# Performance work log

Measured on AMD Instinct MI355X. Metric: run time of the kernel, lower is better.

Reference implementation:

```python
import jax, jax.numpy as jnp
import numpy as np

HIDDEN = 2048
NUM_HEADS = 16
HEAD_DIM = HIDDEN // NUM_HEADS  # 128
LATENT = HIDDEN // 8            # 256
ROPE_THETA = 100000.0


def setup_inputs() -> dict:
    key = jax.random.key(0)
    ks = jax.random.split(key, 7)
    s = 0.02
    x = jax.random.normal(ks[0], (4, 1024, HIDDEN), dtype=jnp.float32)
    # weights stored as [in, out] (transpose of torch nn.Linear.weight)
    w_q_down = jax.random.normal(ks[1], (HIDDEN, LATENT), dtype=jnp.float32) * s
    w_kv_down = jax.random.normal(ks[2], (HIDDEN, LATENT), dtype=jnp.float32) * s
    w_q_up = jax.random.normal(ks[3], (LATENT, HIDDEN), dtype=jnp.float32) * s
    w_k_up = jax.random.normal(ks[4], (LATENT, HIDDEN), dtype=jnp.float32) * s
    w_v_up = jax.random.normal(ks[5], (LATENT, HIDDEN), dtype=jnp.float32) * s
    w_o = jax.random.normal(ks[6], (HIDDEN, HIDDEN), dtype=jnp.float32) * s
    return {"x": x, "w_q_down": w_q_down, "w_kv_down": w_kv_down,
            "w_q_up": w_q_up, "w_k_up": w_k_up, "w_v_up": w_v_up, "w_o": w_o}


def _rope_cos_sin(seq_len, dtype):
    # Llama rotary: inv_freq over even dims, emb = concat(freqs, freqs)
    inv_freq = 1.0 / (ROPE_THETA ** (jnp.arange(0, HEAD_DIM, 2, dtype=jnp.float32) / HEAD_DIM))
    pos = jnp.arange(seq_len, dtype=jnp.float32)
    freqs = pos[:, None] * inv_freq[None, :]          # [S, D/2]
    emb = jnp.concatenate([freqs, freqs], axis=-1)    # [S, D]
    return jnp.cos(emb).astype(dtype), jnp.sin(emb).astype(dtype)


def _rotate_half(t):
    h = t.shape[-1] // 2
    return jnp.concatenate([-t[..., h:], t[..., :h]], axis=-1)


def reference(x, w_q_down, w_kv_down, w_q_up, w_k_up, w_v_up, w_o):
    B, S, H = x.shape
    q_latent = x @ w_q_down                 # [B,S,latent]
    kv_latent = x @ w_kv_down               # [B,S,latent]
    q = (q_latent @ w_q_up).reshape(B, S, NUM_HEADS, HEAD_DIM)
    k = (kv_latent @ w_k_up).reshape(B, S, NUM_HEADS, HEAD_DIM)
    v = (kv_latent @ w_v_up).reshape(B, S, NUM_HEADS, HEAD_DIM)

    cos, sin = _rope_cos_sin(S, x.dtype)    # [S,D]
    cos = cos[None, :, None, :]             # [1,S,1,D] (unsqueeze_dim=2)
    sin = sin[None, :, None, :]
    q = q * cos + _rotate_half(q) * sin
    k = k * cos + _rotate_half(k) * sin

    # [B,H,S,D]
    q = q.transpose(0, 2, 1, 3)
    k = k.transpose(0, 2, 1, 3)
    v = v.transpose(0, 2, 1, 3)

    scale = 1.0 / jnp.sqrt(jnp.asarray(HEAD_DIM, dtype=x.dtype))
    scores = jnp.einsum('bhqd,bhkd->bhqk', q, k) * scale
    causal = jnp.tril(jnp.ones((S, S), dtype=bool))
    scores = jnp.where(causal[None, None], scores, jnp.finfo(scores.dtype).min)
    probs = jax.nn.softmax(scores, axis=-1)
    attn = jnp.einsum('bhqk,bhkd->bhqd', probs, v)  # [B,H,S,D]
    attn = attn.transpose(0, 2, 1, 3).reshape(B, S, H)
    return attn @ w_o
```

## Files before the change

kernel.cpp:

```cpp
#include <hip/hip_runtime.h>
#include <hip/hip_bf16.h>

typedef unsigned short u16;
typedef unsigned int u32;
typedef __attribute__((ext_vector_type(8))) __bf16 bf16x8;
typedef __attribute__((ext_vector_type(4))) float f32x4;

#define HID 2048
#define NH 16
#define HD 128
#define LAT 256
#define BATCH 4
#define SEQ 1024

__device__ __forceinline__ u16 f2bf(float f) {
  union { float f; u32 u; } v; v.f = f;
  u32 r = v.u + 0x7fffu + ((v.u >> 16) & 1u);
  return (u16)(r >> 16);
}

typedef const __attribute__((address_space(1))) u32 as1_u32;
typedef __attribute__((address_space(3))) u32 as3_u32;

__device__ __forceinline__ void load_lds16(const void* g, void* l) {
  __builtin_amdgcn_global_load_lds((as1_u32*)g, (as3_u32*)l, 16, 0, 0);
}

template<int WM, int WN, int MR, int NR>
__device__ __forceinline__ void gemm_core(const u16* __restrict__ A, const u16* __restrict__ Bt,
    int K, int lda, int ldb, int arow0, int brow0, u16* As, u16* Bs, f32x4 acc[MR][NR]) {
  constexpr int BM = WM * MR * 16, BN = WN * NR * 16;
  constexpr int NW = WM * WN;
  constexpr int ACH = (BM * 32) / 512;
  constexpr int BCH = (BN * 32) / 512;
  const int tid = threadIdx.x;
  const int lane = tid & 63, wave = tid >> 6;
  const int wm = wave % WM, wn = wave / WM;
  const int fr = lane & 15, fq = lane >> 4;

  for (int kt = 0; kt < K; kt += 32) {
    __syncthreads();
    #pragma unroll
    for (int cc = 0; cc < ACH / NW; ++cc) {
      int c = wave + cc * NW;
      int r = c * 16 + (lane >> 2);
      int col = (lane & 3) * 8;
      load_lds16(&A[(size_t)(arow0 + r) * lda + kt + col], &As[c * 512]);
    }
    #pragma unroll
    for (int cc = 0; cc < BCH / NW; ++cc) {
      int c = wave + cc * NW;
      int r = c * 16 + (lane >> 2);
      int col = (lane & 3) * 8;
      load_lds16(&Bt[(size_t)(brow0 + r) * ldb + kt + col], &Bs[c * 512]);
    }
    asm volatile("s_waitcnt vmcnt(0)" ::: "memory");
    __syncthreads();
    bf16x8 af[MR], bfr[NR];
    #pragma unroll
    for (int m = 0; m < MR; ++m)
      af[m] = *(const bf16x8*)&As[(wm * MR * 16 + m * 16 + fr) * 32 + fq * 8];
    #pragma unroll
    for (int n = 0; n < NR; ++n)
      bfr[n] = *(const bf16x8*)&Bs[(wn * NR * 16 + n * 16 + fr) * 32 + fq * 8];
    #pragma unroll
    for (int m = 0; m < MR; ++m)
      #pragma unroll
      for (int n = 0; n < NR; ++n)
        acc[m][n] = __builtin_amdgcn_mfma_f32_16x16x32_bf16(af[m], bfr[n], acc[m][n], 0, 0, 0);
  }
}

__global__ void __launch_bounds__(256) k_cvt(const float* __restrict__ in, u16* __restrict__ o, int n4) {
  int i = blockIdx.x * blockDim.x + threadIdx.x;
  if (i < n4) {
    float4 v = ((const float4*)in)[i];
    union { u16 s[4]; uint2 u; } w;
    w.s[0] = f2bf(v.x); w.s[1] = f2bf(v.y); w.s[2] = f2bf(v.z); w.s[3] = f2bf(v.w);
    ((uint2*)o)[i] = w.u;
  }
}

__global__ void __launch_bounds__(256) k_transpose3(const float* __restrict__ in0,
    const float* __restrict__ in1, const float* __restrict__ in2,
    u16* __restrict__ o0, u16* __restrict__ o1, u16* __restrict__ o2, int R, int C) {
  __shared__ float t[32][33];
  const float* in = blockIdx.z == 0 ? in0 : (blockIdx.z == 1 ? in1 : in2);
  u16* o = blockIdx.z == 0 ? o0 : (blockIdx.z == 1 ? o1 : o2);
  int bx = blockIdx.x * 32, by = blockIdx.y * 32;
  int tx = threadIdx.x, ty = threadIdx.y;
  #pragma unroll
  for (int i = ty; i < 32; i += 8) t[i][tx] = in[(size_t)(by + i) * C + bx + tx];
  __syncthreads();
  #pragma unroll
  for (int i = ty; i < 32; i += 8) o[(size_t)(bx + i) * R + by + tx] = f2bf(t[tx][i]);
}

__global__ void __launch_bounds__(256) k_cossin(float* __restrict__ cosT, float* __restrict__ sinT) {
  int idx = blockIdx.x * 256 + threadIdx.x;
  int s = idx >> 6, d = idx & 63;
  float inv = powf(100000.0f, -(float)d / 64.0f);
  float a = (float)s * inv;
  cosT[idx] = cosf(a);
  sinT[idx] = sinf(a);
}

__global__ void __launch_bounds__(512, 2) k_down(const u16* __restrict__ xb, const u16* __restrict__ wqdT,
    const u16* __restrict__ wkvdT, u16* __restrict__ ql, u16* __restrict__ kvl) {
  __shared__ __align__(16) u16 As[2][128 * 128];
  __shared__ __align__(16) u16 Bs[2][64 * 128];
  const u16* Bt = blockIdx.z ? wkvdT : wqdT;
  u16* out = blockIdx.z ? kvl : ql;
  const int rb = blockIdx.x * 128, cb = blockIdx.y * 64;
  const int tid = threadIdx.x, lane = tid & 63, wave = tid >> 6;
  const int wm = wave & 3, wn = wave >> 2;
  const int fr = lane & 15, fq = lane >> 4;
  const char* Ab = (const char*)xb;
  const char* Bb = (const char*)Bt;
  f32x4 acc[2][2] = {};

  auto stage = [&](int buf, int s) {
    #pragma unroll
    for (int cc = 0; cc < 4; ++cc) {
      int c = wave * 4 + cc;
      int L = c * 1024 + lane * 16;
      int Ls = L ^ (((L >> 8) & 7) << 4);
      int r = Ls >> 8, colb = Ls & 255;
      load_lds16(Ab + (size_t)(rb + r) * 4096 + s * 256 + colb, (char*)As[buf] + c * 1024);
    }
    #pragma unroll
    for (int cc = 0; cc < 2; ++cc) {
      int c = wave * 2 + cc;
      int L = c * 1024 + lane * 16;
      int Ls = L ^ (((L >> 8) & 7) << 4);
      int r = Ls >> 8, colb = Ls & 255;
      load_lds16(Bb + (size_t)(cb + r) * 4096 + s * 256 + colb, (char*)Bs[buf] + c * 1024);
    }
  };

  stage(0, 0);
  int buf = 0;
  for (int s = 0; s < 16; ++s) {
    if (s + 1 < 16) {
      stage(buf ^ 1, s + 1);
      asm volatile("s_waitcnt vmcnt(6)" ::: "memory");
    } else {
      asm volatile("s_waitcnt vmcnt(0)" ::: "memory");
    }
    asm volatile("s_barrier" ::: "memory");

    #pragma unroll
    for (int kk = 0; kk < 4; ++kk) {
      bf16x8 af[2], bfr[2];
      #pragma unroll
      for (int m = 0; m < 2; ++m) {
        int r = wm * 32 + m * 16 + fr;
        af[m] = *(const bf16x8*)((const char*)As[buf] + ((r * 256 + kk * 64 + fq * 16) ^ ((r & 7) << 4)));
      }
      #pragma unroll
      for (int n = 0; n < 2; ++n) {
        int r = wn * 32 + n * 16 + fr;
        bfr[n] = *(const bf16x8*)((const char*)Bs[buf] + ((r * 256 + kk * 64 + fq * 16) ^ ((r & 7) << 4)));
      }
      #pragma unroll
      for (int m = 0; m < 2; ++m)
        #pragma unroll
        for (int n = 0; n < 2; ++n)
          acc[m][n] = __builtin_amdgcn_mfma_f32_16x16x32_bf16(af[m], bfr[n], acc[m][n], 0, 0, 0);
    }

    asm volatile("s_barrier" ::: "memory");
    buf ^= 1;
  }

  #pragma unroll
  for (int m = 0; m < 2; ++m)
    #pragma unroll
    for (int n = 0; n < 2; ++n)
      #pragma unroll
      for (int i = 0; i < 4; ++i)
        out[(size_t)(rb + wm * 32 + m * 16 + fq * 4 + i) * LAT + cb + wn * 32 + n * 16 + fr] =
            f2bf(acc[m][n][i]);
}

__global__ void __launch_bounds__(256) k_up(const u16* __restrict__ ql, const u16* __restrict__ kvl,
    const u16* __restrict__ wquT, const u16* __restrict__ wkuT, const u16* __restrict__ wvuT,
    u16* __restrict__ q, u16* __restrict__ k, u16* __restrict__ vt,
    const float* __restrict__ cosT, const float* __restrict__ sinT) {
  __shared__ __align__(16) u16 As[128 * 32];
  __shared__ __align__(16) u16 Bs[128 * 32];
  const int mode = blockIdx.z;
  const u16* A = (mode == 0) ? ql : kvl;
  const u16* Bt = (mode == 0) ? wquT : (mode == 1 ? wkuT : wvuT);
  const int rb = blockIdx.x * 128;
  const int h = blockIdx.y;
  f32x4 acc[2][8] = {};
  gemm_core<4, 1, 2, 8>(A, Bt, LAT, LAT, LAT, rb, h * HD, As, Bs, acc);
  const int lane = threadIdx.x & 63, wave = threadIdx.x >> 6;
  const int fr = lane & 15, fq = lane >> 4;
  if (mode == 2) {
    #pragma unroll
    for (int m = 0; m < 2; ++m)
      #pragma unroll
      for (int n = 0; n < 8; ++n)
        #pragma unroll
        for (int i = 0; i < 4; ++i) {
          int row = rb + wave * 32 + m * 16 + fq * 4 + i;
          int b = row >> 10, s = row & 1023;
          int sp = (s & ~63) | (((s & 15) << 2) | ((s >> 4) & 3));
          vt[(size_t)((b * NH + h) * HD + n * 16 + fr) * SEQ + sp] = f2bf(acc[m][n][i]);
        }
  } else {
    u16* dst = (mode == 0) ? q : k;
    const float scale = (mode == 0) ? 0.08838834764831845f * 1.4426950408889634f : 1.0f;
    #pragma unroll
    for (int m = 0; m < 2; ++m)
      #pragma unroll
      for (int i = 0; i < 4; ++i) {
        int row = rb + wave * 32 + m * 16 + fq * 4 + i;
        int b = row >> 10, s = row & 1023;
        size_t base = (size_t)((b * NH + h) * SEQ + s) * HD;
        #pragma unroll
        for (int j = 0; j < 4; ++j) {
          int dlo = j * 16 + fr;
          float c = cosT[s * 64 + dlo], sn = sinT[s * 64 + dlo];
          float x1 = acc[m][j][i], x2 = acc[m][j + 4][i];
          dst[base + dlo] = f2bf((x1 * c - x2 * sn) * scale);
          dst[base + dlo + 64] = f2bf((x2 * c + x1 * sn) * scale);
        }
      }
  }
}

__global__ void __launch_bounds__(256, 2) k_attn(const u16* __restrict__ Q, const u16* __restrict__ Kc,
    const u16* __restrict__ Vt, u16* __restrict__ O) {
  __shared__ __align__(16) u16 Ks[2][64 * 128];
  __shared__ __align__(16) u16 Vs[2][128 * 64];
  __shared__ __align__(16) u16 Ps[4][32 * 64];
  const int f = blockIdx.x;
  const int j = (f < 256) ? (7 - (f >> 6)) : ((f - 256) >> 6);
  const int bh = (f & 7) * 8 + ((f >> 3) & 7);
  const int h = bh & (NH - 1), b = bh >> 4;
  const int tid = threadIdx.x, lane = tid & 63, wave = tid >> 6;
  const int fr = lane & 15, fq = lane >> 4;
  const int qw = j * 128 + wave * 32;
  const size_t qkb = (size_t)bh * SEQ * HD;
  const char* Kbase = (const char*)Kc + qkb * 2;
  const char* Vbase = (const char*)Vt + (size_t)bh * HD * SEQ * 2;
  const int nkt = 2 * j + 2;

  auto stage = [&](int buf, int kt) {
    #pragma unroll
    for (int cc = 0; cc < 4; ++cc) {
      int c = wave * 4 + cc;
      int L = c * 1024 + lane * 16;
      int Lk = L ^ (((L >> 8) & 7) << 4);
      load_lds16(Kbase + (size_t)kt * 16384 + Lk, (char*)Ks[buf] + c * 1024);
      int Lv = L ^ (((L >> 7) & 7) << 4);
      int rv = Lv >> 7, colb = Lv & 127;
      load_lds16(Vbase + (size_t)rv * (SEQ * 2) + (size_t)kt * 128 + colb, (char*)Vs[buf] + c * 1024);
    }
  };

  bf16x8 ones;
  #pragma unroll
  for (int z = 0; z < 8; ++z) ones[z] = (__bf16)1.0f;

  bf16x8 qf[2][4];
  #pragma unroll
  for (int m = 0; m < 2; ++m)
    #pragma unroll
    for (int c = 0; c < 4; ++c)
      qf[m][c] = *(const bf16x8*)&Q[qkb + (size_t)(qw + m * 16 + fr) * HD + c * 32 + fq * 8];

  f32x4 ao[2][8] = {};
  f32x4 lacc[2] = {};

  stage(0, 0);

  int cur = 0;
  for (int t = 0; t < nkt; ++t) {
    if (t + 1 < nkt) {
      stage(cur ^ 1, t + 1);
      asm volatile("s_waitcnt vmcnt(8)" ::: "memory");
    } else {
      asm volatile("s_waitcnt vmcnt(0)" ::: "memory");
    }
    asm volatile("s_barrier" ::: "memory");

    const int k0 = t * 64;
    if (k0 <= qw + 31) {
      f32x4 sc[2][4] = {};
      __builtin_amdgcn_s_setprio(1);
      #pragma unroll
      for (int c = 0; c < 4; ++c)
        #pragma unroll
        for (int n = 0; n < 4; ++n) {
          int rr = n * 16 + fr;
          int off = (rr * 256 + c * 64 + fq * 16) ^ ((rr & 7) << 4);
          bf16x8 kf = *(const bf16x8*)((const char*)Ks[cur] + off);
          #pragma unroll
          for (int m = 0; m < 2; ++m)
            sc[m][n] = __builtin_amdgcn_mfma_f32_16x16x32_bf16(qf[m][c], kf, sc[m][n], 0, 0, 0);
        }
      __builtin_amdgcn_s_setprio(0);

      bf16x8 pa[2][2];
      #pragma unroll
      for (int m = 0; m < 2; ++m) {
        const bool needmask = (k0 + 63 > qw + m * 16);
        #pragma unroll
        for (int i = 0; i < 4; ++i) {
          int row = qw + m * 16 + fq * 4 + i;
          float p[4];
          #pragma unroll
          for (int n = 0; n < 4; ++n) {
            float sv = sc[m][n][i];
            if (needmask) sv = (k0 + n * 16 + fr <= row) ? sv : -1e30f;
            p[n] = exp2f(sv);
          }
          u32 w0, w1;
          asm("v_cvt_pk_bf16_f32 %0, %1, %2" : "=v"(w0) : "v"(p[0]), "v"(p[1]));
          asm("v_cvt_pk_bf16_f32 %0, %1, %2" : "=v"(w1) : "v"(p[2]), "v"(p[3]));
          int prow = m * 16 + fq * 4 + i;
          int o = (prow * 128 + fr * 8) ^ ((prow & 7) << 4);
          *(uint2*)((char*)Ps[wave] + o) = make_uint2(w0, w1);
        }
        #pragma unroll
        for (int kf = 0; kf < 2; ++kf) {
          int rr = m * 16 + fr;
          int off = (rr * 128 + kf * 64 + fq * 16) ^ ((rr & 7) << 4);
          pa[m][kf] = *(const bf16x8*)((const char*)Ps[wave] + off);
        }
      }

      __builtin_amdgcn_s_setprio(1);
      #pragma unroll
      for (int m = 0; m < 2; ++m) {
        lacc[m] = __builtin_amdgcn_mfma_f32_16x16x32_bf16(pa[m][0], ones, lacc[m], 0, 0, 0);
        lacc[m] = __builtin_amdgcn_mfma_f32_16x16x32_bf16(pa[m][1], ones, lacc[m], 0, 0, 0);
      }
      #pragma unroll
      for (int jj = 0; jj < 8; ++jj)
        #pragma unroll
        for (int kf = 0; kf < 2; ++kf) {
          int rv = jj * 16 + fr;
          int off = (rv * 128 + kf * 64 + fq * 16) ^ ((rv & 7) << 4);
          bf16x8 vf = *(const bf16x8*)((const char*)Vs[cur] + off);
          #pragma unroll
          for (int m = 0; m < 2; ++m)
            ao[m][jj] = __builtin_amdgcn_mfma_f32_16x16x32_bf16(pa[m][kf], vf, ao[m][jj], 0, 0, 0);
        }
      __builtin_amdgcn_s_setprio(0);
    }
    asm volatile("s_barrier" ::: "memory");
    cur ^= 1;
  }

  #pragma unroll
  for (int m = 0; m < 2; ++m)
    #pragma unroll
    for (int i = 0; i < 4; ++i) {
      float inv = 1.f / lacc[m][i];
      int s = qw + m * 16 + fq * 4 + i;
      size_t base = (size_t)(b * SEQ + s) * HID + h * HD;
      #pragma unroll
      for (int jj = 0; jj < 8; ++jj)
        O[base + jj * 16 + fr] = f2bf(ao[m][jj][i] * inv);
    }
}

__global__ void __launch_bounds__(256) k_out(const u16* __restrict__ at, const u16* __restrict__ woT,
    float* __restrict__ out) {
  __shared__ __align__(16) u16 As[128 * 128];
  __shared__ __align__(16) u16 Bs[128 * 128];
  const int rb = blockIdx.x * 128, cb = blockIdx.y * 128;
  const int tid = threadIdx.x, lane = tid & 63, wave = tid >> 6;
  const int wm = wave & 1, wn = wave >> 1;
  const int fr = lane & 15, fq = lane >> 4;
  const char* Ab = (const char*)at;
  const char* Bb = (const char*)woT;

  f32x4 acc[4][4] = {};

  for (int kt = 0; kt < HID; kt += 128) {
    __syncthreads();
    #pragma unroll
    for (int cc = 0; cc < 8; ++cc) {
      int c = wave * 8 + cc;
      int L = c * 1024 + lane * 16;
      int Ls = L ^ (((L >> 8) & 7) << 4);
      int r = Ls >> 8, colb = Ls & 255;
      load_lds16(Ab + (size_t)(rb + r) * (HID * 2) + kt * 2 + colb, (char*)As + c * 1024);
      load_lds16(Bb + (size_t)(cb + r) * (HID * 2) + kt * 2 + colb, (char*)Bs + c * 1024);
    }
    asm volatile("s_waitcnt vmcnt(0)" ::: "memory");
    __syncthreads();

    #pragma unroll
    for (int kk = 0; kk < 4; ++kk) {
      bf16x8 af[4], bfr[4];
      #pragma unroll
      for (int m = 0; m < 4; ++m) {
        int r = wm * 64 + m * 16 + fr;
        af[m] = *(const bf16x8*)((const char*)As + ((r * 256 + kk * 64 + fq * 16) ^ ((r & 7) << 4)));
      }
      #pragma unroll
      for (int n = 0; n < 4; ++n) {
        int r = wn * 64 + n * 16 + fr;
        bfr[n] = *(const bf16x8*)((const char*)Bs + ((r * 256 + kk * 64 + fq * 16) ^ ((r & 7) << 4)));
      }
      #pragma unroll
      for (int m = 0; m < 4; ++m)
        #pragma unroll
        for (int n = 0; n < 4; ++n)
          acc[m][n] = __builtin_amdgcn_mfma_f32_16x16x32_bf16(af[m], bfr[n], acc[m][n], 0, 0, 0);
    }
  }

  #pragma unroll
  for (int m = 0; m < 4; ++m)
    #pragma unroll
    for (int n = 0; n < 4; ++n)
      #pragma unroll
      for (int i = 0; i < 4; ++i)
        out[(size_t)(rb + wm * 64 + m * 16 + fq * 4 + i) * HID + cb + wn * 64 + n * 16 + fr] =
            acc[m][n][i];
}

extern "C" void kernel_launch(void* const* d_in, const int* in_sizes, int n_in,
                              void* d_out, int out_size, void* d_ws, size_t ws_size,
                              hipStream_t stream) {
  const float* x    = (const float*)d_in[0];
  const float* wqd  = (const float*)d_in[1];
  const float* wkvd = (const float*)d_in[2];
  const float* wqu  = (const float*)d_in[3];
  const float* wku  = (const float*)d_in[4];
  const float* wvu  = (const float*)d_in[5];
  const float* wo   = (const float*)d_in[6];
  float* out = (float*)d_out;

  char* p = (char*)d_ws;
  u16* xb    = (u16*)(p + 0);
  u16* at    = xb;
  u16* wqdT  = (u16*)(p + 16777216);
  u16* wkvdT = (u16*)(p + 17825792);
  u16* wquT  = (u16*)(p + 18874368);
  u16* wkuT  = (u16*)(p + 19922944);
  u16* wvuT  = (u16*)(p + 20971520);
  u16* woT   = (u16*)(p + 22020096);
  u16* ql    = (u16*)(p + 30408704);
  u16* kvl   = (u16*)(p + 32505856);
  u16* q     = (u16*)(p + 34603008);
  u16* kk    = (u16*)(p + 51380224);
  u16* vt    = (u16*)(p + 68157440);
  float* cosT = (float*)(p + 84934656);
  float* sinT = (float*)(p + 85196800);

  k_cvt<<<8192, 256, 0, stream>>>(x, xb, 2097152);
  k_transpose3<<<dim3(8, 64, 2), dim3(32, 8), 0, stream>>>(wqd, wkvd, wkvd, wqdT, wkvdT, wkvdT, 2048, 256);
  k_transpose3<<<dim3(64, 8, 3), dim3(32, 8), 0, stream>>>(wqu, wku, wvu, wquT, wkuT, wvuT, 256, 2048);
  k_transpose3<<<dim3(64, 64, 1), dim3(32, 8), 0, stream>>>(wo, wo, wo, woT, woT, woT, 2048, 2048);
  k_cossin<<<256, 256, 0, stream>>>(cosT, sinT);

  k_down<<<dim3(32, 4, 2), 512, 0, stream>>>(xb, wqdT, wkvdT, ql, kvl);
  k_up<<<dim3(32, 16, 3), 256, 0, stream>>>(ql, kvl, wquT, wkuT, wvuT, q, kk, vt, cosT, sinT);
  k_attn<<<512, 256, 0, stream>>>(q, kk, vt, at);
  k_out<<<dim3(32, 16), 256, 0, stream>>>(at, woT, out);
}
```

Measured before the change: 159.0 us.

## Compute transposed scores to keep P in registers, dropping LDS round-trip

Swaps the MFMA operands so the score tile comes out transposed: each lane holds a column of keys for one query row. The probabilities can then be packed straight into the A-operand fragment for the PV MFMA, with no store to a per-wave LDS buffer and reload. V's sequence permutation in the up-projection epilogue is changed to match the new k ordering. The block-to-(j, bh) mapping is also reworked, and the Ps shared buffer is removed, freeing LDS.

```diff
diff --git a/kernel.cpp b/kernel.cpp
--- a/kernel.cpp
+++ b/kernel.cpp
@@ -207,7 +207,8 @@
         for (int i = 0; i < 4; ++i) {
           int row = rb + wave * 32 + m * 16 + fq * 4 + i;
           int b = row >> 10, s = row & 1023;
-          int sp = (s & ~63) | (((s & 15) << 2) | ((s >> 4) & 3));
+          int sp = (s & ~63) | (((s >> 4) & 1) << 5) | (((s >> 3) & 1) << 4) |
+                   (((s >> 2) & 1) << 3) | (((s >> 5) & 1) << 2) | (s & 3);
           vt[(size_t)((b * NH + h) * HD + n * 16 + fr) * SEQ + sp] = f2bf(acc[m][n][i]);
         }
   } else {
@@ -236,10 +237,9 @@
     const u16* __restrict__ Vt, u16* __restrict__ O) {
   __shared__ __align__(16) u16 Ks[2][64 * 128];
   __shared__ __align__(16) u16 Vs[2][128 * 64];
-  __shared__ __align__(16) u16 Ps[4][32 * 64];
   const int f = blockIdx.x;
-  const int j = (f < 256) ? (7 - (f >> 6)) : ((f - 256) >> 6);
-  const int bh = (f & 7) * 8 + ((f >> 3) & 7);
+  const int j = 7 - ((f >> 5) & 7);
+  const int bh = (f & 7) * 8 + ((f >> 3) & 3) + (((f >> 8) & 1) << 2);
   const int h = bh & (NH - 1), b = bh >> 4;
   const int tid = threadIdx.x, lane = tid & 63, wave = tid >> 6;
   const int fr = lane & 15, fq = lane >> 4;
@@ -301,7 +301,7 @@
           bf16x8 kf = *(const bf16x8*)((const char*)Ks[cur] + off);
           #pragma unroll
           for (int m = 0; m < 2; ++m)
-            sc[m][n] = __builtin_amdgcn_mfma_f32_16x16x32_bf16(qf[m][c], kf, sc[m][n], 0, 0, 0);
+            sc[m][n] = __builtin_amdgcn_mfma_f32_16x16x32_bf16(kf, qf[m][c], sc[m][n], 0, 0, 0);
         }
       __builtin_amdgcn_s_setprio(0);
 
@@ -309,28 +309,27 @@
       #pragma unroll
       for (int m = 0; m < 2; ++m) {
         const bool needmask = (k0 + 63 > qw + m * 16);
-        #pragma unroll
-        for (int i = 0; i < 4; ++i) {
-          int row = qw + m * 16 + fq * 4 + i;
-          float p[4];
+        const int qrow = qw + m * 16 + fr;
+        float p[4][4];
+        #pragma unroll
+        for (int n = 0; n < 4; ++n)
           #pragma unroll
-          for (int n = 0; n < 4; ++n) {
+          for (int i = 0; i < 4; ++i) {
             float sv = sc[m][n][i];
-            if (needmask) sv = (k0 + n * 16 + fr <= row) ? sv : -1e30f;
-            p[n] = exp2f(sv);
+            if (needmask) {
+              int kg = k0 + n * 16 + fq * 4 + i;
+              sv = (kg <= qrow) ? sv : -1e30f;
+            }
+            p[n][i] = exp2f(sv);
           }
-          u32 w0, w1;
-          asm("v_cvt_pk_bf16_f32 %0, %1, %2" : "=v"(w0) : "v"(p[0]), "v"(p[1]));
-          asm("v_cvt_pk_bf16_f32 %0, %1, %2" : "=v"(w1) : "v"(p[2]), "v"(p[3]));
-          int prow = m * 16 + fq * 4 + i;
-          int o = (prow * 128 + fr * 8) ^ ((prow & 7) << 4);
-          *(uint2*)((char*)Ps[wave] + o) = make_uint2(w0, w1);
-        }
         #pragma unroll
         for (int kf = 0; kf < 2; ++kf) {
-          int rr = m * 16 + fr;
-          int off = (rr * 128 + kf * 64 + fq * 16) ^ ((rr & 7) << 4);
-          pa[m][kf] = *(const bf16x8*)((const char*)Ps[wave] + off);
+          union { bf16x8 v; u32 w[4]; } pu;
+          asm("v_cvt_pk_bf16_f32 %0, %1, %2" : "=v"(pu.w[0]) : "v"(p[kf][0]), "v"(p[kf][1]));
+          asm("v_cvt_pk_bf16_f32 %0, %1, %2" : "=v"(pu.w[1]) : "v"(p[kf][2]), "v"(p[kf][3]));
+          asm("v_cvt_pk_bf16_f32 %0, %1, %2" : "=v"(pu.w[2]) : "v"(p[2 + kf][0]), "v"(p[2 + kf][1]));
+          asm("v_cvt_pk_bf16_f32 %0, %1, %2" : "=v"(pu.w[3]) : "v"(p[2 + kf][2]), "v"(p[2 + kf][3]));
+          pa[m][kf] = pu.v;
         }
       }
 
```

After: 161.8 us. About the same (+1.8%).
